# Kernel optimization log

Measured on AMD Instinct MI355X. Metric: run time of the kernel, lower is better.

The kernel has to match this reference:

```python
import jax, jax.numpy as jnp
import numpy as np

EPS = 1e-5

def bn(x, p, axis):
    # p: (4,C) = [gamma, beta, running_mean, running_var]; eval-mode batchnorm
    g, b, m, v = p
    shp = [1] * x.ndim
    shp[axis] = -1
    g = g.reshape(shp); b = b.reshape(shp); m = m.reshape(shp); v = v.reshape(shp)
    return (x - m) * g * jax.lax.rsqrt(v + EPS) + b

def knn_idx(query, ref, k):
    # query (B,S,D), ref (B,N,D) -> (B,S,k) nearest-neighbor indices
    d = (jnp.sum(query * query, -1)[:, :, None]
         - 2.0 * jnp.einsum('bsd,bnd->bsn', query, ref)
         + jnp.sum(ref * ref, -1)[:, None, :])
    return jax.lax.top_k(-d, k)[1]

def fps(xyz, npoint):
    # farthest point sampling, deterministic start at index 0. xyz (B,N,3) -> (B,npoint)
    B, N, _ = xyz.shape
    def body(i, state):
        idxs, dists, far = state
        idxs = idxs.at[:, i].set(far)
        centroid = jnp.take_along_axis(xyz, far[:, None, None], axis=1)  # (B,1,3)
        d = jnp.sum((xyz - centroid) ** 2, -1)                           # (B,N)
        dists = jnp.minimum(dists, d)
        return idxs, dists, jnp.argmax(dists, -1).astype(jnp.int32)
    idxs = jnp.zeros((B, npoint), jnp.int32)
    dists = jnp.full((B, N), 1e10, xyz.dtype)
    far = jnp.zeros((B,), jnp.int32)
    idxs, _, _ = jax.lax.fori_loop(0, npoint, body, (idxs, dists, far))
    return idxs

def sample_and_group(npoint, nsample, xyz, feature):
    # xyz (B,N,3); feature (B,C,N) channel-first -> new_xyz (B,S,3), new_feature (B,S,k,2C)
    B = xyz.shape[0]
    xyz_sg = jax.lax.stop_gradient(xyz)
    fps_idx = fps(xyz_sg, npoint)                       # (B,S)
    bi = jnp.arange(B)[:, None]
    new_xyz = xyz[bi, fps_idx]                          # (B,S,3)
    ft = jnp.swapaxes(feature, 1, 2)                    # (B,N,C)
    new_pts = ft[bi, fps_idx]                           # (B,S,C)
    idx = knn_idx(jax.lax.stop_gradient(new_xyz), xyz_sg, nsample)  # (B,S,k)
    grouped = ft[jnp.arange(B)[:, None, None], idx]     # (B,S,k,C)
    centered = grouped - new_pts[:, :, None, :]
    new_feature = jnp.concatenate(
        [centered, jnp.broadcast_to(new_pts[:, :, None, :], grouped.shape)], -1)
    return new_xyz, new_feature

def local_op(x, w, bnp):
    # x (B,S,k,D); conv1d k=1 over D, bn, relu, max over neighbors -> (B,out,S)
    h = jax.nn.relu(bn(jnp.einsum('bskd,od->bsko', x, w), bnp, -1))
    return jnp.swapaxes(jnp.max(h, axis=2), 1, 2)

def edge_branch(f_t, idx, w, bnp):
    # DGCNN-style EdgeConv: concat(f_j - f_i, f_i), conv2d k=1, bn, leakyrelu, max over k
    B = f_t.shape[0]
    nb = f_t[jnp.arange(B)[:, None, None], idx]         # (B,N,k,C)
    center = jnp.broadcast_to(f_t[:, :, None, :], nb.shape)
    e = jnp.concatenate([nb - center, center], -1)      # (B,N,k,2C)
    h = jax.nn.leaky_relu(bn(jnp.einsum('bnkc,oc->bnko', e, w), bnp, -1), 0.2)
    return jnp.max(h, axis=2)                           # (B,N,C)

def dual_graph_fusion(xyz_cf, f, k, geo_w, geo_bn, feat_w, feat_bn, fuse_w, fuse_bn):
    # xyz_cf (B,3,N), f (B,C,N): one kNN graph in coordinate space, one in feature space,
    # EdgeConv on each, concat, 1x1 conv fusion -> (B,C,N)
    xyz_t = jax.lax.stop_gradient(jnp.swapaxes(xyz_cf, 1, 2))  # (B,N,3)
    f_t = jnp.swapaxes(f, 1, 2)                                # (B,N,C)
    idx_g = knn_idx(xyz_t, xyz_t, k)
    f_sg = jax.lax.stop_gradient(f_t)
    idx_f = knn_idx(f_sg, f_sg, k)
    g = edge_branch(f_t, idx_g, geo_w, geo_bn)
    h = edge_branch(f_t, idx_f, feat_w, feat_bn)
    fused = jnp.concatenate([g, h], -1)                        # (B,N,2C)
    out = jax.nn.leaky_relu(bn(jnp.einsum('bnc,oc->bno', fused, fuse_w), fuse_bn, -1), 0.2)
    return jnp.swapaxes(out, 1, 2)                             # (B,C,N)

def _bn_params(key, c):
    k1, k2, k3, k4 = jax.random.split(key, 4)
    g = jax.random.uniform(k1, (c,), minval=0.5, maxval=1.5)
    b = jax.random.normal(k2, (c,)) * 0.1
    m = jax.random.normal(k3, (c,)) * 0.1
    v = jax.random.uniform(k4, (c,), minval=0.5, maxval=1.5)
    return jnp.stack([g, b, m, v])

def setup_inputs() -> dict:
    key = jax.random.key(0)
    ks = jax.random.split(key, 20)
    B, N = 16, 2048
    def w(k, o, i):
        return jax.random.normal(k, (o, i), dtype=jnp.float32) * (1.0 / np.sqrt(i))
    return {
        'x': jax.random.normal(ks[0], (B, 6, N), dtype=jnp.float32),
        'w1': w(ks[1], 64, 6),        'bn1': _bn_params(ks[2], 64),
        'w2': w(ks[3], 1024, 64),     'bn2': _bn_params(ks[4], 1024),
        'geo_w': w(ks[5], 64, 128),   'geo_bn': _bn_params(ks[6], 64),
        'feat_w': w(ks[7], 64, 128),  'feat_bn': _bn_params(ks[8], 64),
        'fuse_w': w(ks[9], 64, 128),  'fuse_bn': _bn_params(ks[10], 64),
        'gl0_w': w(ks[11], 128, 128), 'gl0_bn': _bn_params(ks[12], 128),
        'gl1_w': w(ks[13], 256, 256), 'gl1_bn': _bn_params(ks[14], 256),
        'wf': w(ks[15], 512, 1280),   'bnf': _bn_params(ks[16], 512),
    }

def reference(x, w1, bn1, w2, bn2, geo_w, geo_bn, feat_w, feat_bn, fuse_w, fuse_bn,
              gl0_w, gl0_bn, gl1_w, gl1_bn, wf, bnf):
    B, _, N = x.shape
    xyz = jnp.swapaxes(x[:, 0:3, :], 1, 2)                                   # (B,N,3)
    f_o = jax.nn.relu(bn(jnp.einsum('bcn,oc->bon', x, w1), bn1, 1))          # (B,64,N)
    out_feat = dual_graph_fusion(x[:, 0:3, :], f_o, 20,
                                 geo_w, geo_bn, feat_w, feat_bn, fuse_w, fuse_bn)
    stride = N // 256
    x_skip = jax.nn.relu(bn(jnp.einsum('bcn,oc->bon', f_o[:, :, ::stride], w2), bn2, 1))  # (B,1024,256)
    new_xyz, nf = sample_and_group(512, 32, xyz, out_feat)
    f0 = local_op(nf, gl0_w, gl0_bn)                                         # (B,128,512)
    new_xyz, nf = sample_and_group(256, 32, new_xyz, f0)
    f1 = local_op(nf, gl1_w, gl1_bn)                                         # (B,256,256)
    f1 = jnp.concatenate([f1, x_skip], 1)                                    # (B,1280,256)
    res = jax.nn.leaky_relu(bn(jnp.einsum('bcn,oc->bon', f1, wf), bnf, 1), 0.2)  # (B,512,256)
    return res
```

## Files before the change

### kernel.cpp

```cpp
#include <hip/hip_runtime.h>
#include <float.h>
#include <math.h>


static constexpr int B_   = 16;
static constexpr int N_   = 2048;
static constexpr int NP1  = 512;
static constexpr int NP2  = 256;
static constexpr int KG   = 20;
static constexpr int NSAMP= 32;
static constexpr int CHQ  = 256;

static constexpr long OFF_FT   = 0;
static constexpr long OFF_SQ   = OFF_FT   + (long)B_*N_*64;
static constexpr long OFF_BIG  = OFF_SQ   + (long)B_*N_;
static constexpr long OFF_IDXG = OFF_BIG  + (long)B_*N_*256;
static constexpr long OFF_IDXF = OFF_IDXG + (long)B_*N_*KG;
static constexpr long OFF_OUTF = OFF_IDXF + (long)B_*N_*KG;
static constexpr long OFF_FPS1 = OFF_OUTF + (long)B_*N_*64;
static constexpr long OFF_NX1  = OFF_FPS1 + (long)B_*NP1;
static constexpr long OFF_IDX1 = OFF_NX1  + (long)B_*NP1*3;
static constexpr long OFF_F0T  = OFF_IDX1 + (long)B_*NP1*NSAMP;
static constexpr long OFF_FPS2 = OFF_F0T  + (long)B_*NP1*128;
static constexpr long OFF_NX2  = OFF_FPS2 + (long)B_*NP2;
static constexpr long OFF_IDX2 = OFF_NX2  + (long)B_*NP2*3;
static constexpr long OFF_Q1   = OFF_IDX2 + (long)B_*NP2*NSAMP;
static constexpr long OFF_V    = OFF_Q1   + (long)B_*NP1*512;
static constexpr long OFF_WPP  = OFF_V    + (long)B_*NP2*1280;
static constexpr long OFF_WPQ0 = OFF_WPP  + 256*64;
static constexpr long OFF_WPQ1 = OFF_WPQ0 + 256*64;
static constexpr long OFF_WFT  = OFF_WPQ1 + 512*128;
static constexpr long OFF_SC   = OFF_WFT  + 128*64;
static constexpr long OFF_DL1  = OFF_SC   + 4352;
static constexpr long OFF_DL2  = OFF_DL1  + (long)B_*256*8;
static constexpr long OFF_ST   = OFF_DL2  + (long)B_*512;
static constexpr long OFF_XYZ4 = OFF_ST   + 256;

static constexpr int SC_S1=0, SC_T1=64, SC_SGEO=128, SC_TGEO=192, SC_SFEAT=256, SC_TFEAT=320,
   SC_SFUSE=384, SC_TFUSE=448, SC_SGL0=512, SC_TGL0=640, SC_SGL1=768, SC_TGL1=1024,
   SC_S2=1280, SC_T2=2304, SC_SF=3328, SC_TF=3840;

__device__ __forceinline__ float lrelu_(float x) { return x >= 0.0f ? x : 0.2f * x; }

template<int CTRL, int RM>
__device__ __forceinline__ float dpp_maxm(float v) {
    int o = __builtin_amdgcn_update_dpp(__float_as_int(v), __float_as_int(v),
                                        CTRL, RM, 0xF, false);
    return fmaxf(v, __int_as_float(o));
}
__device__ __forceinline__ float wave_max64_sgpr(float v) {
    v = dpp_maxm<0xB1, 0xF>(v);
    v = dpp_maxm<0x4E, 0xF>(v);
    v = dpp_maxm<0x141,0xF>(v);
    v = dpp_maxm<0x140,0xF>(v);
    v = dpp_maxm<0x142,0xA>(v);
    v = dpp_maxm<0x143,0xC>(v);
    return __int_as_float(__builtin_amdgcn_readlane(__float_as_int(v), 63));
}

template<int CTRL, int RM>
__device__ __forceinline__ unsigned dpp_minm(unsigned x) {
    unsigned o = (unsigned)__builtin_amdgcn_update_dpp((int)x, (int)x, CTRL, RM, 0xF, false);
    return o < x ? o : x;
}
__device__ __forceinline__ unsigned wave_minu_sgpr(unsigned x) {
    x = dpp_minm<0xB1, 0xF>(x);
    x = dpp_minm<0x4E, 0xF>(x);
    x = dpp_minm<0x141,0xF>(x);
    x = dpp_minm<0x140,0xF>(x);
    x = dpp_minm<0x142,0xA>(x);
    x = dpp_minm<0x143,0xC>(x);
    return (unsigned)__builtin_amdgcn_readlane((int)x, 63);
}

__device__ __forceinline__ unsigned sortable_(float f) {
    unsigned u = __float_as_uint(f);
    return u ^ ((unsigned)((int)u >> 31) | 0x80000000u);
}

__device__ __forceinline__ void prep_body(
    const float* bn1, const float* bn2,
    const float* geow, const float* geobn,
    const float* featw, const float* featbn,
    const float* fusew, const float* fusebn,
    const float* gl0w, const float* gl0bn,
    const float* gl1w, const float* gl1bn,
    const float* bnfp, float* ws, int bid)
{
    const int tid = bid * 256 + threadIdx.x;
    const int nt  = 64 * 256;
    float* sc = ws + OFF_SC;
    {
        const float* ps[8]  = {bn1, geobn, featbn, fusebn, gl0bn, gl1bn, bn2, bnfp};
        const int    ch[8]  = {64, 64, 64, 64, 128, 256, 1024, 512};
        const int    so[8]  = {SC_S1, SC_SGEO, SC_SFEAT, SC_SFUSE, SC_SGL0, SC_SGL1, SC_S2, SC_SF};
        const int    to[8]  = {SC_T1, SC_TGEO, SC_TFEAT, SC_TFUSE, SC_TGL0, SC_TGL1, SC_T2, SC_TF};
        for (int g = 0; g < 8; g++) {
            const float* p = ps[g]; int C = ch[g];
            for (int i = tid; i < C; i += nt) {
                float gg = p[i], bb = p[C+i], mm = p[2*C+i], vv = p[3*C+i];
                float s = gg * (1.0f / sqrtf(vv + 1e-5f));
                sc[so[g] + i] = s;
                sc[to[g] + i] = bb - mm * s;
            }
        }
    }
    for (int j = tid; j < 256*64; j += nt) {
        int o = j >> 6, c = j & 63; float v;
        if      (o < 64)  v = geow[o*128 + c];
        else if (o < 128) v = geow[(o-64)*128 + 64 + c];
        else if (o < 192) v = featw[(o-128)*128 + c];
        else              v = featw[(o-192)*128 + 64 + c];
        ws[OFF_WPP + j] = v;
    }
    for (int j = tid; j < 256*64; j += nt) {
        int o = j >> 6, c = j & 63; float v;
        if (o < 128) v = gl0w[o*128 + c];
        else         v = gl0w[(o-128)*128 + 64 + c] - gl0w[(o-128)*128 + c];
        ws[OFF_WPQ0 + j] = v;
    }
    for (int j = tid; j < 512*128; j += nt) {
        int o = j >> 7, c = j & 127; float v;
        if (o < 256) v = gl1w[o*256 + c];
        else         v = gl1w[(o-256)*256 + 128 + c] - gl1w[(o-256)*256 + c];
        ws[OFF_WPQ1 + j] = v;
    }
    for (int j = tid; j < 128*64; j += nt) {
        int c = j >> 6, o = j & 63;
        ws[OFF_WFT + j] = fusew[o*128 + c];
    }
}

__device__ __forceinline__ void feat0_body(
    const float* __restrict__ x, const float* __restrict__ w1,
    const float* __restrict__ bn1,
    float* __restrict__ ft, float* __restrict__ sq,
    float4* __restrict__ xyz4, int bid)
{
    const int t = threadIdx.x, lane = t & 63, w = t >> 6;
    const int pid = bid*4 + w;
    const int b = pid >> 11, n = pid & (N_-1);
    const float* xb = x + (long)b*6*N_ + n;
    float acc = 0.0f;
    #pragma unroll
    for (int c = 0; c < 6; c++) acc += w1[lane*6 + c] * xb[(long)c*N_];
    float gg = bn1[lane], bb = bn1[64+lane], mm = bn1[128+lane], vv = bn1[192+lane];
    float s = gg * (1.0f / sqrtf(vv + 1e-5f));
    float tt = bb - mm * s;
    float val = fmaxf(s*acc + tt, 0.0f);
    ft[((long)b*N_ + n)*64 + lane] = val;
    float v2 = val*val;
    #pragma unroll
    for (int sft = 1; sft < 64; sft <<= 1) v2 += __shfl_xor(v2, sft);
    if (lane == 0) {
        sq[b*N_ + n] = v2;
        float rx = xb[0], ry = xb[N_], rz = xb[2*N_];
        float g2 = __fadd_rn(__fadd_rn(__fmul_rn(rx,rx), __fmul_rn(ry,ry)), __fmul_rn(rz,rz));
        xyz4[(long)b*N_ + n] = make_float4(rx, ry, rz, g2);
    }
}

__global__ void __launch_bounds__(256) k_init(
    const float* __restrict__ x, const float* __restrict__ w1,
    const float* bn1, const float* bn2,
    const float* geow, const float* geobn,
    const float* featw, const float* featbn,
    const float* fusew, const float* fusebn,
    const float* gl0w, const float* gl0bn,
    const float* gl1w, const float* gl1bn,
    const float* bnfp, float* ws,
    float* __restrict__ ft, float* __restrict__ sq, float4* __restrict__ xyz4)
{
    if (blockIdx.x < 64u) {
        prep_body(bn1, bn2, geow, geobn, featw, featbn, fusew, fusebn,
                  gl0w, gl0bn, gl1w, gl1bn, bnfp, ws, blockIdx.x);
        return;
    }
    feat0_body(x, w1, bn1, ft, sq, xyz4, blockIdx.x - 64);
}

template<int RPL, int KSEL>
__device__ __forceinline__ void topk_sel4(float (&v)[RPL], int lane, int* __restrict__ out)
{
    unsigned key[RPL];
    #pragma unroll
    for (int j = 0; j < RPL; j++) key[j] = sortable_(v[j]);

    unsigned consumed = 0;
    unsigned m1 = 0xFFFFFFFFu, m2 = 0xFFFFFFFFu, m3 = 0xFFFFFFFFu;
    int s1 = 0, s2 = 0, s3 = 0;
    #pragma unroll
    for (int j = 0; j < RPL; j++) {
        unsigned kk = key[j];
        bool lt1 = kk < m1, lt2 = kk < m2, lt3 = kk < m3;
        unsigned nm3 = lt2 ? m2 : (lt3 ? kk : m3);
        int      ns3 = lt2 ? s2 : (lt3 ? j  : s3);
        unsigned nm2 = lt1 ? m1 : (lt2 ? kk : m2);
        int      ns2 = lt1 ? s1 : (lt2 ? j  : s2);
        m1 = lt1 ? kk : m1;
        s1 = lt1 ? j  : s1;
        m2 = nm2; s2 = ns2; m3 = nm3; s3 = ns3;
    }

    int keep = 0;
    #pragma unroll 1
    for (int k = 0; k < KSEL; k++) {
        unsigned g = wave_minu_sgpr(m1);
        unsigned long long cand = __ballot(m1 == g);
        int gi;
        if (__popcll(cand) > 1) {
            int ci = (m1 == g) ? (s1*64 + lane) : 0x7FFFFFFF;
            #pragma unroll
            for (int s = 1; s < 64; s <<= 1) { int o = __shfl_xor(ci, s); ci = o < ci ? o : ci; }
            gi = ci;
        } else {
            int wl = __ffsll((long long)cand) - 1;
            gi = __builtin_amdgcn_readlane(s1, wl) * 64 + wl;
        }
        keep = (lane == k) ? gi : keep;
        if (k + 1 < KSEL) {
            bool win = (m1 == g) && (s1*64 + lane == gi);
            if (win) {
                consumed |= 1u << s1;
                m1 = m2; s1 = s2;
                m2 = m3; s2 = s3;
                m3 = 0xFFFFFFFFu;
            }
            bool need = win && (m1 == 0xFFFFFFFFu);
            if (__any(need)) {
                if (need) {
                    m1 = 0xFFFFFFFFu; m2 = 0xFFFFFFFFu; m3 = 0xFFFFFFFFu;
                    s1 = 0; s2 = 0; s3 = 0;
                    #pragma unroll
                    for (int j = 0; j < RPL; j++) {
                        unsigned kk = ((consumed >> j) & 1u) ? 0xFFFFFFFFu : key[j];
                        bool lt1 = kk < m1, lt2 = kk < m2, lt3 = kk < m3;
                        unsigned nm3 = lt2 ? m2 : (lt3 ? kk : m3);
                        int      ns3 = lt2 ? s2 : (lt3 ? j  : s3);
                        unsigned nm2 = lt1 ? m1 : (lt2 ? kk : m2);
                        int      ns2 = lt1 ? s1 : (lt2 ? j  : s2);
                        m1 = lt1 ? kk : m1;
                        s1 = lt1 ? j  : s1;
                        m2 = nm2; s2 = ns2; m3 = nm3; s3 = ns3;
                    }
                }
            }
        }
    }
    if (lane < KSEL) out[lane] = keep;
}

template<int RPL, int KSEL, bool QX4>
__device__ __forceinline__ void knn_x4body(
    const float4* __restrict__ xyz4, int NQ,
    const float* __restrict__ qp, long qBatch, int qsN,
    int* __restrict__ out, int bid)
{
    const int t = threadIdx.x, lane = t & 63, w = t >> 6;
    const int bpb = NQ / 4;
    const int b = bid / bpb;
    const int qi = (bid % bpb)*4 + w;
    const float4* rb = xyz4 + (long)b*N_;
    float qx, qy, qz, sumq;
    if constexpr (QX4) {
        float4 q = rb[qi];
        qx = q.x; qy = q.y; qz = q.z; sumq = q.w;
    } else {
        const float* qb = qp + (long)b*qBatch + (long)qi*qsN;
        qx = qb[0]; qy = qb[1]; qz = qb[2];
        sumq = __fadd_rn(__fadd_rn(__fmul_rn(qx,qx), __fmul_rn(qy,qy)), __fmul_rn(qz,qz));
    }
    float v[RPL];
    #pragma unroll
    for (int j = 0; j < RPL; j++) {
        float4 r = rb[j*64 + lane];
        float dot = __fadd_rn(__fadd_rn(__fmul_rn(qx,r.x), __fmul_rn(qy,r.y)), __fmul_rn(qz,r.z));
        v[j] = __fadd_rn(__fsub_rn(sumq, __fmul_rn(2.0f, dot)), r.w);
    }
    topk_sel4<RPL, KSEL>(v, lane, out + ((long)b*NQ + qi)*KSEL);
}

template<int RPL, int KSEL>
__device__ __forceinline__ void knn_gbody(
    const float* qp, long qBatch, int qsN, int NQ,
    const float* rp, long rBatch, int rsN,
    int* out, int bid)
{
    const int t = threadIdx.x, lane = t & 63, w = t >> 6;
    const int bpb = NQ / 4;
    const int b = bid / bpb;
    const int qi = (bid % bpb)*4 + w;
    const float* rb = rp + (long)b*rBatch;
    const float* qb = qp + (long)b*qBatch + (long)qi*qsN;
    float qx = qb[0], qy = qb[1], qz = qb[2];
    float sumq = __fadd_rn(__fadd_rn(__fmul_rn(qx,qx), __fmul_rn(qy,qy)), __fmul_rn(qz,qz));
    float v[RPL];
    #pragma unroll
    for (int j = 0; j < RPL; j++) {
        long n = j*64 + lane;
        float rx = rb[n*rsN], ry = rb[n*rsN + 1], rz = rb[n*rsN + 2];
        float dot = __fadd_rn(__fadd_rn(__fmul_rn(qx,rx), __fmul_rn(qy,ry)), __fmul_rn(qz,rz));
        float sumr = __fadd_rn(__fadd_rn(__fmul_rn(rx,rx), __fmul_rn(ry,ry)), __fmul_rn(rz,rz));
        v[j] = __fadd_rn(__fsub_rn(sumq, __fmul_rn(2.0f, dot)), sumr);
    }
    topk_sel4<RPL, KSEL>(v, lane, out + ((long)b*NQ + qi)*KSEL);
}

__device__ __forceinline__ void fps1_seg_body(
    const float* __restrict__ x, int b, int i0, int cnt,
    int* __restrict__ fps1, float* __restrict__ nx1,
    float* __restrict__ dl1s, float* __restrict__ st, float* __restrict__ smem)
{
    __builtin_amdgcn_s_setprio(3);
    const int t = threadIdx.x, lane = t & 63, wave = t >> 6;
    const float* pb = x + (long)b*6*N_;

    float4* mrgc   = (float4*)smem;
    int*    mrgi   = (int*)(smem + 32);
    int*    sidxsg = (int*)(smem + 40);
    float*  mxsg   = smem + 296;
    float*  mysg   = smem + 552;
    float*  mzsg   = smem + 808;

    float px[8], py[8], pz[8], dl[8];
    {
        const float4* a4  = (const float4*)(pb + 8*t);
        const float4* b4  = (const float4*)(pb + N_ + 8*t);
        const float4* c4p = (const float4*)(pb + 2*N_ + 8*t);
        float4 a0 = a4[0], a1 = a4[1];
        float4 b0 = b4[0], b1 = b4[1];
        float4 c0 = c4p[0], c1 = c4p[1];
        px[0]=a0.x; px[1]=a0.y; px[2]=a0.z; px[3]=a0.w;
        px[4]=a1.x; px[5]=a1.y; px[6]=a1.z; px[7]=a1.w;
        py[0]=b0.x; py[1]=b0.y; py[2]=b0.z; py[3]=b0.w;
        py[4]=b1.x; py[5]=b1.y; py[6]=b1.z; py[7]=b1.w;
        pz[0]=c0.x; pz[1]=c0.y; pz[2]=c0.z; pz[3]=c0.w;
        pz[4]=c1.x; pz[5]=c1.y; pz[6]=c1.z; pz[7]=c1.w;
    }
    int far; float cx, cy, cz;
    if (i0 == 0) {
        #pragma unroll
        for (int p = 0; p < 8; p++) dl[p] = 1e10f;
        far = 0; cx = pb[0]; cy = pb[N_]; cz = pb[2*N_];
    } else {
        const float4* ds = (const float4*)(dl1s + ((long)b*256 + t)*8);
        float4 d0 = ds[0], d1 = ds[1];
        dl[0]=d0.x; dl[1]=d0.y; dl[2]=d0.z; dl[3]=d0.w;
        dl[4]=d1.x; dl[5]=d1.y; dl[6]=d1.z; dl[7]=d1.w;
        far = __float_as_int(st[b*16+0]);
        cx = st[b*16+1]; cy = st[b*16+2]; cz = st[b*16+3];
    }

    for (int k = 0; k < cnt; k++) {
        if (t == 0) { sidxsg[k] = far; mxsg[k] = cx; mysg[k] = cy; mzsg[k] = cz; }
        float bv = -1.0f; int bp = 0;
        #pragma unroll
        for (int p = 0; p < 8; p++) {
            float dx = __fsub_rn(px[p], cx);
            float dy = __fsub_rn(py[p], cy);
            float dz = __fsub_rn(pz[p], cz);
            float d  = __fadd_rn(__fadd_rn(__fmul_rn(dx,dx), __fmul_rn(dy,dy)), __fmul_rn(dz,dz));
            float nd = fminf(dl[p], d);
            dl[p] = nd;
            if (nd > bv) { bv = nd; bp = p; }
        }
        float wx = px[0], wy = py[0], wz = pz[0];
        #pragma unroll
        for (int p = 1; p < 8; p++) {
            bool c = (bp == p);
            wx = c ? px[p] : wx; wy = c ? py[p] : wy; wz = c ? pz[p] : wz;
        }
        float gm = wave_max64_sgpr(bv);
        unsigned long long cand = __ballot(bv == gm);
        int wl = __ffsll((long long)cand) - 1;
        int   wbp = __builtin_amdgcn_readlane(bp, wl);
        float sxw = __int_as_float(__builtin_amdgcn_readlane(__float_as_int(wx), wl));
        float syw = __int_as_float(__builtin_amdgcn_readlane(__float_as_int(wy), wl));
        float szw = __int_as_float(__builtin_amdgcn_readlane(__float_as_int(wz), wl));
        int par = k & 1;
        if (lane == 0) {
            mrgc[par*4 + wave] = make_float4(sxw, syw, szw, gm);
            mrgi[par*4 + wave] = (((wave << 6) | wl) << 3) + wbp;
        }
        __syncthreads();
        float4 e0 = mrgc[par*4 + 0];
        float fv = e0.w; int fi = mrgi[par*4 + 0];
        float ncx = e0.x, ncy = e0.y, ncz = e0.z;
        #pragma unroll
        for (int w2 = 1; w2 < 4; w2++) {
            float4 e2 = mrgc[par*4 + w2]; int i2 = mrgi[par*4 + w2];
            if (e2.w > fv) { fv = e2.w; fi = i2; ncx = e2.x; ncy = e2.y; ncz = e2.z; }
        }
        far = fi; cx = ncx; cy = ncy; cz = ncz;
    }
    __syncthreads();

    int*   f1o = fps1 + b*NP1;
    float* n1o = nx1 + (long)b*NP1*3;
    for (int s = t; s < cnt; s += 256) {
        f1o[i0+s] = sidxsg[s];
        n1o[(long)(i0+s)*3+0] = mxsg[s];
        n1o[(long)(i0+s)*3+1] = mysg[s];
        n1o[(long)(i0+s)*3+2] = mzsg[s];
    }
    float4* ds = (float4*)(dl1s + ((long)b*256 + t)*8);
    ds[0] = make_float4(dl[0], dl[1], dl[2], dl[3]);
    ds[1] = make_float4(dl[4], dl[5], dl[6], dl[7]);
    if (t == 0) {
        st[b*16+0] = __int_as_float(far);
        st[b*16+1] = cx; st[b*16+2] = cy; st[b*16+3] = cz;
    }
    __builtin_amdgcn_s_setprio(0);
}

__device__ __forceinline__ void fps2_seg_body(
    int b, int i0, int cnt,
    const float* __restrict__ nx1, int* __restrict__ fps2, float* __restrict__ nx2,
    float* __restrict__ dl2s, float* __restrict__ st, float* __restrict__ smem)
{
    __builtin_amdgcn_s_setprio(3);
    const int t = threadIdx.x, lane = t & 63, wave = t >> 6;
    float4* mrgc   = (float4*)smem;
    int*    mrgi   = (int*)(smem + 32);
    int*    sidxsg = (int*)(smem + 40);
    float*  mx2    = smem + 168;
    float*  my2    = smem + 680;
    float*  mz2    = smem + 1192;

    const float* n1 = nx1 + (long)b*NP1*3;
    for (int s = t; s < NP1; s += 256) {
        mx2[s] = n1[(long)s*3+0];
        my2[s] = n1[(long)s*3+1];
        mz2[s] = n1[(long)s*3+2];
    }
    __syncthreads();

    const int n0 = t << 1;
    float ax = mx2[n0],   ay = my2[n0],   az = mz2[n0];
    float bx = mx2[n0+1], by = my2[n0+1], bz = mz2[n0+1];
    float dl0, dl1; int far2; float c2x, c2y, c2z;
    if (i0 == 0) {
        dl0 = dl1 = 1e10f; far2 = 0;
        c2x = mx2[0]; c2y = my2[0]; c2z = mz2[0];
    } else {
        dl0 = dl2s[(long)b*512 + n0];
        dl1 = dl2s[(long)b*512 + n0 + 1];
        far2 = __float_as_int(st[b*16+4]);
        c2x = st[b*16+5]; c2y = st[b*16+6]; c2z = st[b*16+7];
    }

    for (int k = 0; k < cnt; k++) {
        if (t == 0) sidxsg[k] = far2;
        float dx = __fsub_rn(ax, c2x), dy = __fsub_rn(ay, c2y), dz = __fsub_rn(az, c2z);
        float d0 = __fadd_rn(__fadd_rn(__fmul_rn(dx,dx), __fmul_rn(dy,dy)), __fmul_rn(dz,dz));
        dx = __fsub_rn(bx, c2x); dy = __fsub_rn(by, c2y); dz = __fsub_rn(bz, c2z);
        float d1 = __fadd_rn(__fadd_rn(__fmul_rn(dx,dx), __fmul_rn(dy,dy)), __fmul_rn(dz,dz));
        dl0 = fminf(dl0, d0);
        dl1 = fminf(dl1, d1);
        float bv = dl0; int bp = 0;
        if (dl1 > bv) { bv = dl1; bp = 1; }
        float wx = bp ? bx : ax, wy = bp ? by : ay, wz = bp ? bz : az;
        float gm = wave_max64_sgpr(bv);
        unsigned long long cand = __ballot(bv == gm);
        int wl = __ffsll((long long)cand) - 1;
        int   wbp = __builtin_amdgcn_readlane(bp, wl);
        float sxw = __int_as_float(__builtin_amdgcn_readlane(__float_as_int(wx), wl));
        float syw = __int_as_float(__builtin_amdgcn_readlane(__float_as_int(wy), wl));
        float szw = __int_as_float(__builtin_amdgcn_readlane(__float_as_int(wz), wl));
        int par = k & 1;
        if (lane == 0) {
            mrgc[par*4 + wave] = make_float4(sxw, syw, szw, gm);
            mrgi[par*4 + wave] = (((wave << 6) | wl) << 1) + wbp;
        }
        __syncthreads();
        float4 e0 = mrgc[par*4 + 0];
        float fv = e0.w; int fi = mrgi[par*4 + 0];
        float ncx = e0.x, ncy = e0.y, ncz = e0.z;
        #pragma unroll
        for (int w2 = 1; w2 < 4; w2++) {
            float4 e2 = mrgc[par*4 + w2]; int i2 = mrgi[par*4 + w2];
            if (e2.w > fv) { fv = e2.w; fi = i2; ncx = e2.x; ncy = e2.y; ncz = e2.z; }
        }
        far2 = fi; c2x = ncx; c2y = ncy; c2z = ncz;
    }
    __syncthreads();

    int*   f2o = fps2 + b*NP2;
    float* n2o = nx2 + (long)b*NP2*3;
    for (int s = t; s < cnt; s += 256) {
        int j = sidxsg[s];
        f2o[i0+s] = j;
        n2o[(long)(i0+s)*3+0] = mx2[j];
        n2o[(long)(i0+s)*3+1] = my2[j];
        n2o[(long)(i0+s)*3+2] = mz2[j];
    }
    dl2s[(long)b*512 + n0]     = dl0;
    dl2s[(long)b*512 + n0 + 1] = dl1;
    if (t == 0) {
        st[b*16+4] = __int_as_float(far2);
        st[b*16+5] = c2x; st[b*16+6] = c2y; st[b*16+7] = c2z;
    }
    __builtin_amdgcn_s_setprio(0);
}

__device__ __forceinline__ void dist_gemm_body(
    const float* __restrict__ ft, const float* __restrict__ sq,
    float* __restrict__ Dnew, int qbNew, int gi, float* __restrict__ smem)
{
    float* As = smem;
    float* Bs = smem + 4096;
    const int ib = gi & 3;
    const int jb = (gi >> 2) & 31;
    const int b  = gi >> 7;
    const int t  = threadIdx.x;
    const int tx = t & 15, ty = t >> 4;
    const float* Ab = ft + ((long)b*N_ + qbNew + (long)ib*64)*64;
    const float* Bb = ft + ((long)b*N_ + (long)jb*64)*64;
    const float* sqb = sq + (long)b*N_;
    #pragma unroll
    for (int m = 0; m < 4; m++) {
        int li = t + m*256; int r = li >> 4; int c4 = li & 15;
        int cs = r ^ ((c4 & 7) << 2);
        float4 av = *(const float4*)(Ab + (long)r*64 + c4*4);
        As[(c4*4+0)*64 + cs] = av.x; As[(c4*4+1)*64 + cs] = av.y;
        As[(c4*4+2)*64 + cs] = av.z; As[(c4*4+3)*64 + cs] = av.w;
        float4 bv = *(const float4*)(Bb + (long)r*64 + c4*4);
        Bs[(c4*4+0)*64 + cs] = bv.x; Bs[(c4*4+1)*64 + cs] = bv.y;
        Bs[(c4*4+2)*64 + cs] = bv.z; Bs[(c4*4+3)*64 + cs] = bv.w;
    }
    __syncthreads();
    float acc[4][4];
    #pragma unroll
    for (int i = 0; i < 4; i++)
        #pragma unroll
        for (int j = 0; j < 4; j++) acc[i][j] = 0.0f;
    #pragma unroll 4
    for (int k = 0; k < 64; k++) {
        int s4 = ((k >> 2) & 7) << 2;
        float4 a  = *(const float4*)&As[k*64 + ((ty*4) ^ s4)];
        float4 b4 = *(const float4*)&Bs[k*64 + ((tx*4) ^ s4)];
        acc[0][0] += a.x*b4.x; acc[0][1] += a.x*b4.y; acc[0][2] += a.x*b4.z; acc[0][3] += a.x*b4.w;
        acc[1][0] += a.y*b4.x; acc[1][1] += a.y*b4.y; acc[1][2] += a.y*b4.z; acc[1][3] += a.y*b4.w;
        acc[2][0] += a.z*b4.x; acc[2][1] += a.z*b4.y; acc[2][2] += a.z*b4.z; acc[2][3] += a.z*b4.w;
        acc[3][0] += a.w*b4.x; acc[3][1] += a.w*b4.y; acc[3][2] += a.w*b4.z; acc[3][3] += a.w*b4.w;
    }
    const int i0 = ib*64 + ty*4;
    const int j0 = jb*64 + tx*4;
    #pragma unroll
    for (int ii = 0; ii < 4; ii++) {
        float sqq = sqb[qbNew + i0 + ii];
        #pragma unroll
        for (int jj = 0; jj < 4; jj++) {
            int r = j0 + jj;
            Dnew[((long)b*CHQ + i0 + ii)*N_ + r] = (sqq - 2.0f*acc[ii][jj]) + sqb[r];
        }
    }
}

__device__ __forceinline__ void proj64_body(
    int gi, int nIB, int nJB,
    const float* __restrict__ A, long aBatch, int aRow,
    const float* __restrict__ Bw,
    float* __restrict__ C, long cBatch, int cRow, int cCol0,
    int act, const float* __restrict__ sv, const float* __restrict__ tv,
    float* __restrict__ smem)
{
    float* As = smem;
    float* Bs = smem + 4096;
    const int ib = gi % nIB;
    const int jb = (gi / nIB) % nJB;
    const int b  = gi / (nIB*nJB);
    const int t  = threadIdx.x;
    const int tx = t & 15, ty = t >> 4;
    const float* Ab = A + (long)b*aBatch + (long)(ib*64)*aRow;
    #pragma unroll
    for (int m = 0; m < 4; m++) {
        int li = t + m*256; int r = li >> 4; int c4 = li & 15;
        int cs = r ^ ((c4 & 7) << 2);
        float4 av = *(const float4*)(Ab + (long)r*aRow + c4*4);
        As[(c4*4+0)*64 + cs] = av.x; As[(c4*4+1)*64 + cs] = av.y;
        As[(c4*4+2)*64 + cs] = av.z; As[(c4*4+3)*64 + cs] = av.w;
        float4 bv = *(const float4*)(Bw + (long)(jb*64 + r)*64 + c4*4);
        Bs[(c4*4+0)*64 + cs] = bv.x; Bs[(c4*4+1)*64 + cs] = bv.y;
        Bs[(c4*4+2)*64 + cs] = bv.z; Bs[(c4*4+3)*64 + cs] = bv.w;
    }
    __syncthreads();
    float acc[4][4];
    #pragma unroll
    for (int i = 0; i < 4; i++)
        #pragma unroll
        for (int j = 0; j < 4; j++) acc[i][j] = 0.0f;
    #pragma unroll 4
    for (int k = 0; k < 64; k++) {
        int s4 = ((k >> 2) & 7) << 2;
        float4 a  = *(const float4*)&As[k*64 + ((ty*4) ^ s4)];
        float4 b4 = *(const float4*)&Bs[k*64 + ((tx*4) ^ s4)];
        acc[0][0] += a.x*b4.x; acc[0][1] += a.x*b4.y; acc[0][2] += a.x*b4.z; acc[0][3] += a.x*b4.w;
        acc[1][0] += a.y*b4.x; acc[1][1] += a.y*b4.y; acc[1][2] += a.y*b4.z; acc[1][3] += a.y*b4.w;
        acc[2][0] += a.z*b4.x; acc[2][1] += a.z*b4.y; acc[2][2] += a.z*b4.z; acc[2][3] += a.z*b4.w;
        acc[3][0] += a.w*b4.x; acc[3][1] += a.w*b4.y; acc[3][2] += a.w*b4.z; acc[3][3] += a.w*b4.w;
    }
    const int i0 = ib*64 + ty*4;
    const int j0 = jb*64 + tx*4;
    #pragma unroll
    for (int ii = 0; ii < 4; ii++)
        #pragma unroll
        for (int jj = 0; jj < 4; jj++) {
            int j = j0 + jj;
            float vv = acc[ii][jj];
            if (act == 1) vv = fmaxf(sv[j]*vv + tv[j], 0.0f);
            C[(long)b*cBatch + (long)(i0+ii)*cRow + cCol0 + j] = vv;
        }
}

__device__ __forceinline__ void sel_body(
    const float* __restrict__ Dold, int qbOld, int* __restrict__ idxf, int bid)
{
    const int t = threadIdx.x, lane = t & 63, w = t >> 6;
    const int r = bid*4 + w;
    const int b = r >> 8, qi = r & (CHQ-1);
    const float* row = Dold + ((long)b*CHQ + qi) * N_;
    float v[32];
    #pragma unroll
    for (int j = 0; j < 32; j++) v[j] = row[j*64 + lane];
    topk_sel4<32, KG>(v, lane, idxf + ((long)b*N_ + qbOld + qi)*KG);
}

__device__ __forceinline__ void edgefuse_body(
    const float* __restrict__ P, const int* __restrict__ idxg, const int* __restrict__ idxf,
    const float* __restrict__ wft, const float* __restrict__ sc,
    float* __restrict__ outf, int bid, float* __restrict__ smem)
{
    float* wt = smem;
    float* fused = smem + 8192;
    const int t = threadIdx.x, lane = t & 63, w = t >> 6;
    for (int i = t; i < 128*64; i += 256) wt[i] = wft[i];
    const int pid = bid*4 + w;
    const int b = pid >> 11, n = pid & (N_-1);
    const float* Prow = P + ((long)b*N_ + n)*256;
    const int* ig  = idxg + ((long)b*N_ + n)*KG;
    const int* ifx = idxf + ((long)b*N_ + n)*KG;
    float gmax = -FLT_MAX, hmax = -FLT_MAX;
    for (int k = 0; k < KG; k++) {
        int idg = ig[k];
        gmax = fmaxf(gmax, P[((long)b*N_ + idg)*256 + lane]);
        int idf = ifx[k];
        hmax = fmaxf(hmax, P[((long)b*N_ + idf)*256 + 128 + lane]);
    }
    float glin = gmax - Prow[lane]       + Prow[64 + lane];
    float hlin = hmax - Prow[128 + lane] + Prow[192 + lane];
    float gv = lrelu_(sc[SC_SGEO + lane]*glin + sc[SC_TGEO + lane]);
    float hv = lrelu_(sc[SC_SFEAT + lane]*hlin + sc[SC_TFEAT + lane]);
    fused[w*128 + lane]      = gv;
    fused[w*128 + 64 + lane] = hv;
    __syncthreads();
    float acc = 0.0f;
    #pragma unroll 8
    for (int c4 = 0; c4 < 32; c4++) {
        float4 f = *(const float4*)&fused[w*128 + c4*4];
        acc += f.x * wt[(c4*4+0)*64 + lane];
        acc += f.y * wt[(c4*4+1)*64 + lane];
        acc += f.z * wt[(c4*4+2)*64 + lane];
        acc += f.w * wt[(c4*4+3)*64 + lane];
    }
    float ov = lrelu_(sc[SC_SFUSE + lane]*acc + sc[SC_TFUSE + lane]);
    outf[((long)b*N_ + n)*64 + lane] = ov;
}

template<int QN, int ROWW, int CO, int MROWS, int SO>
__device__ __forceinline__ void gathermax_body(
    const float* __restrict__ Q, const int* __restrict__ knn, const int* __restrict__ fpsi,
    const float* __restrict__ sv, const float* __restrict__ tv,
    float* __restrict__ outp, int outRow, int bid)
{
    const int t = threadIdx.x, lane = t & 63, w = t >> 6;
    const int pid = bid*4 + w;
    const int b = pid / SO, s = pid % SO;
    const int* ix = knn + ((long)b*SO + s)*NSAMP;
    float mx[QN];
    #pragma unroll
    for (int q = 0; q < QN; q++) mx[q] = -FLT_MAX;
    for (int k = 0; k < NSAMP; k++) {
        int id = ix[k];
        const float* r = Q + ((long)b*MROWS + id)*ROWW;
        #pragma unroll
        for (int q = 0; q < QN; q++) mx[q] = fmaxf(mx[q], r[lane + 64*q]);
    }
    int crow = fpsi[b*SO + s];
    const float* cr = Q + ((long)b*MROWS + crow)*ROWW + CO;
    #pragma unroll
    for (int q = 0; q < QN; q++) {
        int o = lane + 64*q;
        float lin = mx[q] + cr[o];
        float val = fmaxf(sv[o]*lin + tv[o], 0.0f);
        outp[((long)b*SO + s)*outRow + o] = val;
    }
}

__global__ void __launch_bounds__(256, 4) k_geo0(
    const float* __restrict__ x, const float4* __restrict__ xyz4,
    int* __restrict__ idxg,
    int* __restrict__ fps1, float* __restrict__ nx1,
    float* __restrict__ dl1s, float* __restrict__ st,
    const float* __restrict__ ft, const float* __restrict__ sq,
    float* __restrict__ D0)
{
    __shared__ float smem[8192];
    if (blockIdx.x < (unsigned)B_) {
        fps1_seg_body(x, blockIdx.x, 0, 256, fps1, nx1, dl1s, st, smem);
        return;
    }
    if (blockIdx.x < (unsigned)(B_ + 8192)) {
        knn_x4body<32, KG, true>(xyz4, N_, nullptr, 0, 0, idxg, blockIdx.x - B_);
        return;
    }
    dist_gemm_body(ft, sq, D0, 0, blockIdx.x - (B_ + 8192), smem);
}

__global__ void __launch_bounds__(256, 4) k_chain(
    const float* __restrict__ x, const float* __restrict__ ft, const float* __restrict__ sq,
    float* __restrict__ Dnew, int qbNew,
    const float* __restrict__ Dold, int qbOld,
    int* __restrict__ idxf,
    int* __restrict__ fps1, float* __restrict__ nx1,
    float* __restrict__ dl1s, float* __restrict__ st, int i0)
{
    __shared__ float smem[8192];
    if (blockIdx.x < 16u) {
        fps1_seg_body(x, blockIdx.x, i0, 32, fps1, nx1, dl1s, st, smem);
        return;
    }
    if (blockIdx.x < 1040u) {
        sel_body(Dold, qbOld, idxf, blockIdx.x - 16);
        return;
    }
    dist_gemm_body(ft, sq, Dnew, qbNew, blockIdx.x - 1040, smem);
}

__global__ void __launch_bounds__(256, 4) k_tail9(
    const float* __restrict__ x, const float* __restrict__ ft,
    const float* __restrict__ Dold, int qbOld, int* __restrict__ idxf,
    int* __restrict__ fps1, float* __restrict__ nx1,
    float* __restrict__ dl1s, float* __restrict__ st,
    const float* __restrict__ wpp, float* __restrict__ big)
{
    __shared__ float smem[8192];
    if (blockIdx.x < 16u) {
        fps1_seg_body(x, blockIdx.x, 480, 32, fps1, nx1, dl1s, st, smem);
        return;
    }
    if (blockIdx.x < 1040u) {
        sel_body(Dold, qbOld, idxf, blockIdx.x - 16);
        return;
    }
    proj64_body(blockIdx.x - 1040, 32, 4, ft, (long)N_*64, 64, wpp,
                big, (long)N_*256, 256, 0, 0, nullptr, nullptr, smem);
}

__global__ void __launch_bounds__(256, 4) k_tail10(
    const float* __restrict__ nx1, int* __restrict__ fps2, float* __restrict__ nx2,
    float* __restrict__ dl2s, float* __restrict__ st,
    const float* __restrict__ P, const int* __restrict__ idxg, const int* __restrict__ idxf,
    const float* __restrict__ wft, const float* __restrict__ sc, float* __restrict__ outf,
    const float* __restrict__ ft, const float* __restrict__ w2, float* __restrict__ V)
{
    __shared__ float smem[8704];
    if (blockIdx.x < 16u) {
        fps2_seg_body(blockIdx.x, 0, 128, nx1, fps2, nx2, dl2s, st, smem);
        return;
    }
    if (blockIdx.x < (unsigned)(16 + 8192)) {
        edgefuse_body(P, idxg, idxf, wft, sc, outf, blockIdx.x - 16, smem);
        return;
    }
    proj64_body(blockIdx.x - (16 + 8192), 4, 16, ft, (long)N_*64, 512, w2,
                V, (long)NP2*1280, 1280, 256, 1, sc + SC_S2, sc + SC_T2, smem);
}

__global__ void __launch_bounds__(256, 4) k_tail11(
    const float* __restrict__ nx1, int* __restrict__ fps2, float* __restrict__ nx2,
    float* __restrict__ dl2s, float* __restrict__ st,
    const float4* __restrict__ xyz4, int* __restrict__ idx1,
    const float* __restrict__ outf, const float* __restrict__ wpq0, float* __restrict__ big)
{
    __shared__ float smem[8192];
    if (blockIdx.x < 16u) {
        fps2_seg_body(blockIdx.x, 128, 128, nx1, fps2, nx2, dl2s, st, smem);
        return;
    }
    if (blockIdx.x < (unsigned)(16 + 2048)) {
        knn_x4body<32, 32, false>(xyz4, NP1, nx1, (long)NP1*3, 3, idx1, blockIdx.x - 16);
        return;
    }
    proj64_body(blockIdx.x - (16 + 2048), 32, 4, outf, (long)N_*64, 64, wpq0,
                big, (long)N_*256, 256, 0, 0, nullptr, nullptr, smem);
}

__global__ void __launch_bounds__(256, 4) k_gm0knn2(
    const float* __restrict__ big, const int* __restrict__ idx1, const int* __restrict__ fps1,
    const float* __restrict__ sc, float* __restrict__ f0t,
    const float* __restrict__ nx2, const float* __restrict__ nx1, int* __restrict__ idx2)
{
    if (blockIdx.x < 2048u) {
        gathermax_body<2,256,128,2048,512>(big, idx1, fps1,
            sc + SC_SGL0, sc + SC_TGL0, f0t, 128, blockIdx.x);
        return;
    }
    knn_gbody<8,32>(nx2, (long)NP2*3, 3, NP2,
                    nx1, (long)NP1*3, 3, idx2, blockIdx.x - 2048);
}

__global__ void __launch_bounds__(256) k_gemm(
    const float* __restrict__ A, long aBatch, int aRow,
    const float* __restrict__ Bw, long bBatch, int K,
    float* __restrict__ C, long cBatch, int cRow, int cCol0,
    int act, const float* __restrict__ sv, const float* __restrict__ tv,
    int epi)
{
    __shared__ float As[4096];
    __shared__ float Bs[4096];
    const int b  = blockIdx.z;
    const int ib = blockIdx.x * 64;
    const int jb = blockIdx.y * 64;
    const int t  = threadIdx.x;
    const int tx = t & 15, ty = t >> 4;
    const float* Ab = A + (long)b * aBatch;
    const float* Bb = Bw + (long)b * bBatch;
    float acc[4][4];
    #pragma unroll
    for (int i = 0; i < 4; i++)
        #pragma unroll
        for (int j = 0; j < 4; j++) acc[i][j] = 0.0f;

    for (int kb = 0; kb < K; kb += 64) {
        #pragma unroll
        for (int m = 0; m < 4; m++) {
            int li = t + m*256; int r = li >> 4; int c4 = li & 15;
            int cs = r ^ ((c4 & 7) << 2);
            float4 av = *(const float4*)(Ab + (long)(ib + r)*aRow + kb + c4*4);
            As[(c4*4+0)*64 + cs] = av.x; As[(c4*4+1)*64 + cs] = av.y;
            As[(c4*4+2)*64 + cs] = av.z; As[(c4*4+3)*64 + cs] = av.w;
            float4 bv = *(const float4*)(Bb + (long)(jb + r)*K + kb + c4*4);
            Bs[(c4*4+0)*64 + cs] = bv.x; Bs[(c4*4+1)*64 + cs] = bv.y;
            Bs[(c4*4+2)*64 + cs] = bv.z; Bs[(c4*4+3)*64 + cs] = bv.w;
        }
        __syncthreads();
        #pragma unroll 4
        for (int k = 0; k < 64; k++) {
            int s4 = ((k >> 2) & 7) << 2;
            float4 a  = *(const float4*)&As[k*64 + ((ty*4) ^ s4)];
            float4 b4 = *(const float4*)&Bs[k*64 + ((tx*4) ^ s4)];
            acc[0][0] += a.x*b4.x; acc[0][1] += a.x*b4.y; acc[0][2] += a.x*b4.z; acc[0][3] += a.x*b4.w;
            acc[1][0] += a.y*b4.x; acc[1][1] += a.y*b4.y; acc[1][2] += a.y*b4.z; acc[1][3] += a.y*b4.w;
            acc[2][0] += a.z*b4.x; acc[2][1] += a.z*b4.y; acc[2][2] += a.z*b4.z; acc[2][3] += a.z*b4.w;
            acc[3][0] += a.w*b4.x; acc[3][1] += a.w*b4.y; acc[3][2] += a.w*b4.z; acc[3][3] += a.w*b4.w;
        }
        __syncthreads();
    }

    const int i0 = ib + ty*4;
    const int j0 = jb + tx*4;
    if (epi == 2) {
        #pragma unroll
        for (int ii = 0; ii < 4; ii++)
            #pragma unroll
            for (int jj = 0; jj < 4; jj++) {
                int j = j0 + jj;
                float vv = lrelu_(sv[j]*acc[ii][jj] + tv[j]);
                C[(long)b*cBatch + (long)j*cRow + (i0+ii)] = vv;
            }
    } else {
        #pragma unroll
        for (int ii = 0; ii < 4; ii++)
            #pragma unroll
            for (int jj = 0; jj < 4; jj++) {
                int j = j0 + jj;
                float vv = acc[ii][jj];
                if (act == 1) vv = fmaxf(sv[j]*vv + tv[j], 0.0f);
                else if (act == 2) vv = lrelu_(sv[j]*vv + tv[j]);
                C[(long)b*cBatch + (long)(i0+ii)*cRow + cCol0 + j] = vv;
            }
    }
}

template<int QN, int ROWW, int CO, int MROWS, int SO>
__global__ void __launch_bounds__(256) k_gathermax(
    const float* __restrict__ Q, const int* __restrict__ knn, const int* __restrict__ fpsi,
    const float* __restrict__ sv, const float* __restrict__ tv,
    float* __restrict__ outp, int outRow)
{
    gathermax_body<QN,ROWW,CO,MROWS,SO>(Q, knn, fpsi, sv, tv, outp, outRow, blockIdx.x);
}

extern "C" void kernel_launch(void* const* d_in, const int* in_sizes, int n_in,
                              void* d_out, int out_size, void* d_ws, size_t ws_size,
                              hipStream_t stream)
{
    const float* x      = (const float*)d_in[0];
    const float* w1     = (const float*)d_in[1];
    const float* bn1    = (const float*)d_in[2];
    const float* w2     = (const float*)d_in[3];
    const float* bn2    = (const float*)d_in[4];
    const float* geow   = (const float*)d_in[5];
    const float* geobn  = (const float*)d_in[6];
    const float* featw  = (const float*)d_in[7];
    const float* featbn = (const float*)d_in[8];
    const float* fusew  = (const float*)d_in[9];
    const float* fusebn = (const float*)d_in[10];
    const float* gl0w   = (const float*)d_in[11];
    const float* gl0bn  = (const float*)d_in[12];
    const float* gl1w   = (const float*)d_in[13];
    const float* gl1bn  = (const float*)d_in[14];
    const float* wf     = (const float*)d_in[15];
    const float* bnfp   = (const float*)d_in[16];

    float* ws  = (float*)d_ws;
    float* out = (float*)d_out;

    float* FT   = ws + OFF_FT;
    float* SQ   = ws + OFF_SQ;
    float* BIG  = ws + OFF_BIG;
    int*   IDXG = (int*)(ws + OFF_IDXG);
    int*   IDXF = (int*)(ws + OFF_IDXF);
    float* OUTF = ws + OFF_OUTF;
    int*   FPS1 = (int*)(ws + OFF_FPS1);
    float* NX1  = ws + OFF_NX1;
    int*   IDX1 = (int*)(ws + OFF_IDX1);
    float* F0T  = ws + OFF_F0T;
    int*   FPS2 = (int*)(ws + OFF_FPS2);
    float* NX2  = ws + OFF_NX2;
    int*   IDX2 = (int*)(ws + OFF_IDX2);
    float* Q1B  = ws + OFF_Q1;
    float* V    = ws + OFF_V;
    float* WPP  = ws + OFF_WPP;
    float* WPQ0 = ws + OFF_WPQ0;
    float* WPQ1 = ws + OFF_WPQ1;
    float* WFT  = ws + OFF_WFT;
    float* SC   = ws + OFF_SC;
    float* DL1  = ws + OFF_DL1;
    float* DL2  = ws + OFF_DL2;
    float* ST   = ws + OFF_ST;
    float4* XYZ4 = (float4*)(ws + OFF_XYZ4);

    hipLaunchKernelGGL(k_init, dim3(64 + B_*N_/4), dim3(256), 0, stream,
        x, w1, bn1, bn2, geow, geobn, featw, featbn, fusew, fusebn,
        gl0w, gl0bn, gl1w, gl1bn, bnfp, ws, FT, SQ, XYZ4);

    hipLaunchKernelGGL(k_geo0, dim3(B_ + 8192 + 2048), dim3(256), 0, stream,
        x, XYZ4, IDXG, FPS1, NX1, DL1, ST, FT, SQ, BIG);

    float* bufs[2] = { BIG, Q1B };
    for (int ci = 1; ci < 8; ci++) {
        hipLaunchKernelGGL(k_chain, dim3(16 + 1024 + 2048), dim3(256), 0, stream,
            x, FT, SQ,
            bufs[ci & 1], ci*CHQ,
            bufs[(ci - 1) & 1], (ci - 1)*CHQ,
            IDXF, FPS1, NX1, DL1, ST, 256 + 32*(ci - 1));
    }

    hipLaunchKernelGGL(k_tail9, dim3(16 + 1024 + 2048), dim3(256), 0, stream,
        x, FT, bufs[1], 7*CHQ, IDXF, FPS1, NX1, DL1, ST, WPP, BIG);

    hipLaunchKernelGGL(k_tail10, dim3(16 + 8192 + 1024), dim3(256), 0, stream,
        NX1, FPS2, NX2, DL2, ST,
        BIG, IDXG, IDXF, WFT, SC, OUTF,
        FT, w2, V);

    hipLaunchKernelGGL(k_tail11, dim3(16 + 2048 + 2048), dim3(256), 0, stream,
        NX1, FPS2, NX2, DL2, ST,
        XYZ4, IDX1,
        OUTF, WPQ0, BIG);

    hipLaunchKernelGGL(k_gm0knn2, dim3(2048 + 1024), dim3(256), 0, stream,
        BIG, IDX1, FPS1, SC, F0T, NX2, NX1, IDX2);

    hipLaunchKernelGGL(k_gemm, dim3(NP1/64, 512/64, B_), dim3(256), 0, stream,
        F0T, (long)NP1*128, 128, WPQ1, (long)0, 128,
        Q1B, (long)NP1*512, 512, 0, 0, nullptr, nullptr, 0);

    hipLaunchKernelGGL((k_gathermax<4,512,256,512,256>), dim3(B_*NP2/4), dim3(256), 0, stream,
        Q1B, IDX2, FPS2, SC + SC_SGL1, SC + SC_TGL1, V, 1280);

    hipLaunchKernelGGL(k_gemm, dim3(NP2/64, 512/64, B_), dim3(256), 0, stream,
        V, (long)NP2*1280, 1280, wf, (long)0, 1280,
        out, (long)512*256, 256, 0, 2, SC + SC_SF, SC + SC_TF, 2);

    (void)in_sizes; (void)n_in; (void)out_size; (void)ws_size;
}
```

Measured before the change: 621.5 us.

## Compute feature distance GEMM with split-bf16 MFMA instead of FP32 FMA

The pairwise feature dot-product GEMM behind the kNN distance matrix is moved from a shared-memory FP32 FMA tile loop to bf16 MFMA instructions. Features are split into three bf16 parts (hi/mid/lo) in the init kernel, and six cross-term MFMAs per k-step approximate FP32 accuracy. Operands are loaded straight from global memory with no LDS staging, so the shared memory in the chain kernels shrinks. This costs extra workspace, extra stores in init, and small rounding differences that could change neighbor ordering on near-ties.

New measurement: 700.5 us. +12.7%, slower.

```diff
diff --git a/kernel.cpp b/kernel.cpp
--- a/kernel.cpp
+++ b/kernel.cpp
@@ -35,10 +35,16 @@
 static constexpr long OFF_DL2  = OFF_DL1  + (long)B_*256*8;
 static constexpr long OFF_ST   = OFF_DL2  + (long)B_*512;
 static constexpr long OFF_XYZ4 = OFF_ST   + 256;
+static constexpr long OFF_FTH  = OFF_XYZ4 + (long)B_*N_*4;
+static constexpr long OFF_FTM  = OFF_FTH  + (long)B_*N_*32;
+static constexpr long OFF_FTL  = OFF_FTM  + (long)B_*N_*32;
 
 static constexpr int SC_S1=0, SC_T1=64, SC_SGEO=128, SC_TGEO=192, SC_SFEAT=256, SC_TFEAT=320,
    SC_SFUSE=384, SC_TFUSE=448, SC_SGL0=512, SC_TGL0=640, SC_SGL1=768, SC_TGL1=1024,
    SC_S2=1280, SC_T2=2304, SC_SF=3328, SC_TF=3840;
+
+typedef __attribute__((ext_vector_type(8))) __bf16 bf16x8;
+typedef __attribute__((ext_vector_type(4))) float  f32x4;
 
 __device__ __forceinline__ float lrelu_(float x) { return x >= 0.0f ? x : 0.2f * x; }
 
@@ -76,6 +82,13 @@
 __device__ __forceinline__ unsigned sortable_(float f) {
     unsigned u = __float_as_uint(f);
     return u ^ ((unsigned)((int)u >> 31) | 0x80000000u);
+}
+
+__device__ __forceinline__ unsigned rne_bf16_(float f, float& rounded) {
+    unsigned u = __float_as_uint(f);
+    unsigned r = (u + 0x7FFFu + ((u >> 16) & 1u)) & 0xFFFF0000u;
+    rounded = __uint_as_float(r);
+    return r >> 16;
 }
 
 __device__ __forceinline__ void prep_body(
@@ -135,7 +148,9 @@
     const float* __restrict__ x, const float* __restrict__ w1,
     const float* __restrict__ bn1,
     float* __restrict__ ft, float* __restrict__ sq,
-    float4* __restrict__ xyz4, int bid)
+    float4* __restrict__ xyz4,
+    unsigned short* __restrict__ fth, unsigned short* __restrict__ ftm,
+    unsigned short* __restrict__ ftl, int bid)
 {
     const int t = threadIdx.x, lane = t & 63, w = t >> 6;
     const int pid = bid*4 + w;
@@ -148,7 +163,17 @@
     float s = gg * (1.0f / sqrtf(vv + 1e-5f));
     float tt = bb - mm * s;
     float val = fmaxf(s*acc + tt, 0.0f);
-    ft[((long)b*N_ + n)*64 + lane] = val;
+    const long e = ((long)b*N_ + n)*64 + lane;
+    ft[e] = val;
+    float h, m2, dmy;
+    unsigned hb = rne_bf16_(val, h);
+    float r1 = val - h;
+    unsigned mb = rne_bf16_(r1, m2);
+    float r2 = r1 - m2;
+    unsigned lb = rne_bf16_(r2, dmy);
+    fth[e] = (unsigned short)hb;
+    ftm[e] = (unsigned short)mb;
+    ftl[e] = (unsigned short)lb;
     float v2 = val*val;
     #pragma unroll
     for (int sft = 1; sft < 64; sft <<= 1) v2 += __shfl_xor(v2, sft);
@@ -169,14 +194,16 @@
     const float* gl0w, const float* gl0bn,
     const float* gl1w, const float* gl1bn,
     const float* bnfp, float* ws,
-    float* __restrict__ ft, float* __restrict__ sq, float4* __restrict__ xyz4)
+    float* __restrict__ ft, float* __restrict__ sq, float4* __restrict__ xyz4,
+    unsigned short* __restrict__ fth, unsigned short* __restrict__ ftm,
+    unsigned short* __restrict__ ftl)
 {
     if (blockIdx.x < 64u) {
         prep_body(bn1, bn2, geow, geobn, featw, featbn, fusew, fusebn,
                   gl0w, gl0bn, gl1w, gl1bn, bnfp, ws, blockIdx.x);
         return;
     }
-    feat0_body(x, w1, bn1, ft, sq, xyz4, blockIdx.x - 64);
+    feat0_body(x, w1, bn1, ft, sq, xyz4, fth, ftm, ftl, blockIdx.x - 64);
 }
 
 template<int RPL, int KSEL>
@@ -503,56 +530,56 @@
     __builtin_amdgcn_s_setprio(0);
 }
 
-__device__ __forceinline__ void dist_gemm_body(
-    const float* __restrict__ ft, const float* __restrict__ sq,
-    float* __restrict__ Dnew, int qbNew, int gi, float* __restrict__ smem)
-{
-    float* As = smem;
-    float* Bs = smem + 4096;
+__device__ __forceinline__ void dist_mfma_body(
+    const unsigned short* __restrict__ fth, const unsigned short* __restrict__ ftm,
+    const unsigned short* __restrict__ ftl,
+    const float* __restrict__ sq,
+    float* __restrict__ Dnew, int qbNew, int gi)
+{
     const int ib = gi & 3;
     const int jb = (gi >> 2) & 31;
     const int b  = gi >> 7;
-    const int t  = threadIdx.x;
-    const int tx = t & 15, ty = t >> 4;
-    const float* Ab = ft + ((long)b*N_ + qbNew + (long)ib*64)*64;
-    const float* Bb = ft + ((long)b*N_ + (long)jb*64)*64;
+    const int t = threadIdx.x, lane = t & 63, wave = t >> 6;
+    const int qrow0 = ib*64 + wave*16;
+    const int r0 = jb*64;
+    const long baseQ = ((long)b*N_ + qbNew + qrow0 + (lane & 15))*64 + ((lane >> 4)*8);
+    const long baseR = ((long)b*N_ + r0 + (lane & 15))*64 + ((lane >> 4)*8);
+
+    bf16x8 ah[2], am[2], al[2];
+    #pragma unroll
+    for (int s = 0; s < 2; s++) {
+        ah[s] = *(const bf16x8*)(fth + baseQ + s*32);
+        am[s] = *(const bf16x8*)(ftm + baseQ + s*32);
+        al[s] = *(const bf16x8*)(ftl + baseQ + s*32);
+    }
     const float* sqb = sq + (long)b*N_;
-    #pragma unroll
-    for (int m = 0; m < 4; m++) {
-        int li = t + m*256; int r = li >> 4; int c4 = li & 15;
-        int cs = r ^ ((c4 & 7) << 2);
-        float4 av = *(const float4*)(Ab + (long)r*64 + c4*4);
-        As[(c4*4+0)*64 + cs] = av.x; As[(c4*4+1)*64 + cs] = av.y;
-        As[(c4*4+2)*64 + cs] = av.z; As[(c4*4+3)*64 + cs] = av.w;
-        float4 bv = *(const float4*)(Bb + (long)r*64 + c4*4);
-        Bs[(c4*4+0)*64 + cs] = bv.x; Bs[(c4*4+1)*64 + cs] = bv.y;
-        Bs[(c4*4+2)*64 + cs] = bv.z; Bs[(c4*4+3)*64 + cs] = bv.w;
-    }
-    __syncthreads();
-    float acc[4][4];
-    #pragma unroll
-    for (int i = 0; i < 4; i++)
-        #pragma unroll
-        for (int j = 0; j < 4; j++) acc[i][j] = 0.0f;
-    #pragma unroll 4
-    for (int k = 0; k < 64; k++) {
-        int s4 = ((k >> 2) & 7) << 2;
-        float4 a  = *(const float4*)&As[k*64 + ((ty*4) ^ s4)];
-        float4 b4 = *(const float4*)&Bs[k*64 + ((tx*4) ^ s4)];
-        acc[0][0] += a.x*b4.x; acc[0][1] += a.x*b4.y; acc[0][2] += a.x*b4.z; acc[0][3] += a.x*b4.w;
-        acc[1][0] += a.y*b4.x; acc[1][1] += a.y*b4.y; acc[1][2] += a.y*b4.z; acc[1][3] += a.y*b4.w;
-        acc[2][0] += a.z*b4.x; acc[2][1] += a.z*b4.y; acc[2][2] += a.z*b4.z; acc[2][3] += a.z*b4.w;
-        acc[3][0] += a.w*b4.x; acc[3][1] += a.w*b4.y; acc[3][2] += a.w*b4.z; acc[3][3] += a.w*b4.w;
-    }
-    const int i0 = ib*64 + ty*4;
-    const int j0 = jb*64 + tx*4;
-    #pragma unroll
-    for (int ii = 0; ii < 4; ii++) {
-        float sqq = sqb[qbNew + i0 + ii];
-        #pragma unroll
-        for (int jj = 0; jj < 4; jj++) {
-            int r = j0 + jj;
-            Dnew[((long)b*CHQ + i0 + ii)*N_ + r] = (sqq - 2.0f*acc[ii][jj]) + sqb[r];
+    const int rj = r0 + (lane & 15);
+    const int qr = qrow0 + ((lane >> 4) << 2);
+    float sqq[4];
+    #pragma unroll
+    for (int g2 = 0; g2 < 4; g2++) sqq[g2] = sqb[qbNew + qr + g2];
+
+    #pragma unroll
+    for (int j = 0; j < 4; j++) {
+        f32x4 acc = {0.0f, 0.0f, 0.0f, 0.0f};
+        #pragma unroll
+        for (int s = 0; s < 2; s++) {
+            const long off = baseR + (long)j*16*64 + s*32;
+            bf16x8 bh = *(const bf16x8*)(fth + off);
+            bf16x8 bm = *(const bf16x8*)(ftm + off);
+            bf16x8 bl = *(const bf16x8*)(ftl + off);
+            acc = __builtin_amdgcn_mfma_f32_16x16x32_bf16(ah[s], bh, acc, 0, 0, 0);
+            acc = __builtin_amdgcn_mfma_f32_16x16x32_bf16(ah[s], bm, acc, 0, 0, 0);
+            acc = __builtin_amdgcn_mfma_f32_16x16x32_bf16(am[s], bh, acc, 0, 0, 0);
+            acc = __builtin_amdgcn_mfma_f32_16x16x32_bf16(am[s], bm, acc, 0, 0, 0);
+            acc = __builtin_amdgcn_mfma_f32_16x16x32_bf16(ah[s], bl, acc, 0, 0, 0);
+            acc = __builtin_amdgcn_mfma_f32_16x16x32_bf16(al[s], bh, acc, 0, 0, 0);
+        }
+        const int rr = rj + j*16;
+        float sqr = sqb[rr];
+        #pragma unroll
+        for (int g2 = 0; g2 < 4; g2++) {
+            Dnew[((long)b*CHQ + qr + g2)*N_ + rr] = (sqq[g2] - 2.0f*acc[g2]) + sqr;
         }
     }
 }
@@ -702,10 +729,11 @@
     int* __restrict__ idxg,
     int* __restrict__ fps1, float* __restrict__ nx1,
     float* __restrict__ dl1s, float* __restrict__ st,
-    const float* __restrict__ ft, const float* __restrict__ sq,
-    float* __restrict__ D0)
-{
-    __shared__ float smem[8192];
+    const unsigned short* __restrict__ fth, const unsigned short* __restrict__ ftm,
+    const unsigned short* __restrict__ ftl,
+    const float* __restrict__ sq, float* __restrict__ D0)
+{
+    __shared__ float smem[2048];
     if (blockIdx.x < (unsigned)B_) {
         fps1_seg_body(x, blockIdx.x, 0, 256, fps1, nx1, dl1s, st, smem);
         return;
@@ -714,18 +742,21 @@
         knn_x4body<32, KG, true>(xyz4, N_, nullptr, 0, 0, idxg, blockIdx.x - B_);
         return;
     }
-    dist_gemm_body(ft, sq, D0, 0, blockIdx.x - (B_ + 8192), smem);
+    dist_mfma_body(fth, ftm, ftl, sq, D0, 0, blockIdx.x - (B_ + 8192));
 }
 
 __global__ void __launch_bounds__(256, 4) k_chain(
-    const float* __restrict__ x, const float* __restrict__ ft, const float* __restrict__ sq,
+    const float* __restrict__ x,
+    const unsigned short* __restrict__ fth, const unsigned short* __restrict__ ftm,
+    const unsigned short* __restrict__ ftl,
+    const float* __restrict__ sq,
     float* __restrict__ Dnew, int qbNew,
     const float* __restrict__ Dold, int qbOld,
     int* __restrict__ idxf,
     int* __restrict__ fps1, float* __restrict__ nx1,
     float* __restrict__ dl1s, float* __restrict__ st, int i0)
 {
-    __shared__ float smem[8192];
+    __shared__ float smem[2048];
     if (blockIdx.x < 16u) {
         fps1_seg_body(x, blockIdx.x, i0, 32, fps1, nx1, dl1s, st, smem);
         return;
@@ -734,7 +765,7 @@
         sel_body(Dold, qbOld, idxf, blockIdx.x - 16);
         return;
     }
-    dist_gemm_body(ft, sq, Dnew, qbNew, blockIdx.x - 1040, smem);
+    dist_mfma_body(fth, ftm, ftl, sq, Dnew, qbNew, blockIdx.x - 1040);
 }
 
 __global__ void __launch_bounds__(256, 4) k_tail9(
@@ -941,18 +972,21 @@
     float* DL2  = ws + OFF_DL2;
     float* ST   = ws + OFF_ST;
     float4* XYZ4 = (float4*)(ws + OFF_XYZ4);
+    unsigned short* FTH = (unsigned short*)(ws + OFF_FTH);
+    unsigned short* FTM = (unsigned short*)(ws + OFF_FTM);
+    unsigned short* FTL = (unsigned short*)(ws + OFF_FTL);
 
     hipLaunchKernelGGL(k_init, dim3(64 + B_*N_/4), dim3(256), 0, stream,
         x, w1, bn1, bn2, geow, geobn, featw, featbn, fusew, fusebn,
-        gl0w, gl0bn, gl1w, gl1bn, bnfp, ws, FT, SQ, XYZ4);
+        gl0w, gl0bn, gl1w, gl1bn, bnfp, ws, FT, SQ, XYZ4, FTH, FTM, FTL);
 
     hipLaunchKernelGGL(k_geo0, dim3(B_ + 8192 + 2048), dim3(256), 0, stream,
-        x, XYZ4, IDXG, FPS1, NX1, DL1, ST, FT, SQ, BIG);
+        x, XYZ4, IDXG, FPS1, NX1, DL1, ST, FTH, FTM, FTL, SQ, BIG);
 
     float* bufs[2] = { BIG, Q1B };
     for (int ci = 1; ci < 8; ci++) {
         hipLaunchKernelGGL(k_chain, dim3(16 + 1024 + 2048), dim3(256), 0, stream,
-            x, FT, SQ,
+            x, FTH, FTM, FTL, SQ,
             bufs[ci & 1], ci*CHQ,
             bufs[(ci - 1) & 1], (ci - 1)*CHQ,
             IDXF, FPS1, NX1, DL1, ST, 256 + 32*(ci - 1));
```
